# Optimization experiments

Measured on AMD Instinct MI355X. Metric: run time of the kernel, lower is better.

The kernel has to match this reference:

```python
import jax, jax.numpy as jnp
import numpy as np

B, S, E = 2, 2048, 2048
H, HKV = 16, 4
G = H // HKV
QLR, KVLR = 1024, 512
DN, DR, DV = 128, 64, 128
DQK = DN + DR
EPS = 1.1920929e-07  # torch.finfo(float32).eps, F.rms_norm default


def rms_norm(x):
    return x * jax.lax.rsqrt(jnp.mean(x * x, axis=-1, keepdims=True) + EPS)


def apply_rope(x, cos, sin):
    # x: [B, S, h, D]; pairs are adjacent elements (torch view_as_complex convention)
    x0, x1 = x[..., 0::2], x[..., 1::2]            # [B,S,h,D/2]
    c = cos[None, :, None, :]
    s = sin[None, :, None, :]
    r0 = x0 * c - x1 * s
    r1 = x0 * s + x1 * c
    return jnp.stack([r0, r1], axis=-1).reshape(x.shape)


def setup_inputs() -> dict:
    key = jax.random.key(0)
    ks = jax.random.split(key, 8)
    inv_freq = 1.0 / (10000.0 ** (np.arange(0, DR, 2, dtype=np.float32) / DR))  # [DR/2]
    ang = np.arange(S, dtype=np.float32)[:, None] * inv_freq[None, :]           # [S, DR/2]
    return {
        "x": jax.random.normal(ks[0], (B, S, E), jnp.float32),
        "freqs_cos": jnp.asarray(np.cos(ang), jnp.float32),
        "freqs_sin": jnp.asarray(np.sin(ang), jnp.float32),
        "Wqa": jax.random.normal(ks[1], (QLR, E), jnp.float32) * (E ** -0.5),
        "Wqb": jax.random.normal(ks[2], (H * DQK, QLR), jnp.float32) * (QLR ** -0.5),
        "Wkva": jax.random.normal(ks[3], (KVLR + DR, E), jnp.float32) * (E ** -0.5),
        "Wkvb": jax.random.normal(ks[4], (HKV * (DN + DV), KVLR), jnp.float32) * (KVLR ** -0.5),
        "Wo": jax.random.normal(ks[5], (E, H * DV), jnp.float32) * ((H * DV) ** -0.5),
    }


def reference(x, freqs_cos, freqs_sin, Wqa, Wqb, Wkva, Wkvb, Wo):
    # Q path: low-rank down-proj -> rmsnorm -> up-proj
    q = rms_norm(x @ Wqa.T) @ Wqb.T                       # [B,S,H*DQK]
    q = q.reshape(B, S, H, DQK)
    q_nope, q_rope = q[..., :DN], q[..., DN:]
    q_rope = apply_rope(q_rope, freqs_cos, freqs_sin)
    q = jnp.concatenate([q_nope, q_rope], axis=-1)        # [B,S,H,DQK]

    # KV path: joint down-proj, shared rope key, up-proj of latent
    kv_a = x @ Wkva.T                                     # [B,S,KVLR+DR]
    kv_latent, k_rope = kv_a[..., :KVLR], kv_a[..., KVLR:]
    k_rope = jnp.broadcast_to(k_rope[:, :, None, :], (B, S, HKV, DR))
    k_rope = apply_rope(k_rope, freqs_cos, freqs_sin)     # [B,S,HKV,DR]
    kv = (rms_norm(kv_latent) @ Wkvb.T).reshape(B, S, HKV, DN + DV)
    k_nope, v = kv[..., :DN], kv[..., DN:]
    k = jnp.concatenate([k_nope, k_rope], axis=-1)        # [B,S,HKV,DQK]

    # GQA causal SDPA: group G query heads per kv head
    qg = q.reshape(B, S, HKV, G, DQK)
    scores = jnp.einsum("bsngd,btnd->bngst", qg, k) * (DQK ** -0.5)  # [B,HKV,G,S,S]
    causal = jnp.tril(jnp.ones((S, S), bool))
    scores = jnp.where(causal, scores, jnp.finfo(scores.dtype).min)
    attn = jax.nn.softmax(scores, axis=-1)
    o = jnp.einsum("bngst,btnd->bsngd", attn, v).reshape(B, S, H * DV)
    return o @ Wo.T                                        # [B,S,E]
```

## Files before the change

### kernel.cpp

```cpp
#include <hip/hip_runtime.h>
#include <cstdint>
#include <cstddef>

typedef __attribute__((ext_vector_type(4))) float f32x4;
typedef __attribute__((ext_vector_type(2))) float f32x2;
typedef __attribute__((ext_vector_type(8))) short short8;
typedef __attribute__((ext_vector_type(8))) __bf16 bf16x8;
typedef unsigned short u16;
typedef unsigned int u32;
typedef __attribute__((ext_vector_type(2))) unsigned int u32x2;
typedef __attribute__((ext_vector_type(4))) unsigned short u16x4;
typedef __attribute__((ext_vector_type(2))) unsigned short u16x2;

#define EPS_RMS 1.1920929e-07f

__device__ __forceinline__ u16 f2bf(float f) {
  union { float f; unsigned u; } v; v.f = f;
  unsigned r = v.u + 0x7FFFu + ((v.u >> 16) & 1u);
  return (u16)(r >> 16);
}
__device__ __forceinline__ float b2f(u16 x) {
  union { unsigned u; float f; } v; v.u = ((unsigned)x) << 16;
  return v.f;
}
__device__ __forceinline__ u32 cvt_pk_bf16(float lo, float hi) {
  u32 r;
  asm("v_cvt_pk_bf16_f32 %0, %1, %2" : "=v"(r) : "v"(lo), "v"(hi));
  return r;
}

template <typename V>
__device__ __forceinline__ auto mfma_try(V a, V b, f32x4 c, int)
    -> decltype(__builtin_amdgcn_mfma_f32_16x16x32_bf16(a, b, c, 0, 0, 0)) {
  return __builtin_amdgcn_mfma_f32_16x16x32_bf16(a, b, c, 0, 0, 0);
}
template <typename V>
__device__ __forceinline__ f32x4 mfma_try(V a, V b, f32x4 c, long) {
  return __builtin_amdgcn_mfma_f32_16x16x32_bf16(
      __builtin_bit_cast(bf16x8, a), __builtin_bit_cast(bf16x8, b), c, 0, 0, 0);
}
__device__ __forceinline__ f32x4 mfma_bf16(short8 a, short8 b, f32x4 c) {
  return mfma_try(a, b, c, 0);
}

__device__ __forceinline__ void load_lds16(u16* lds, const u16* g) {
  auto* gp = reinterpret_cast<const __attribute__((address_space(1))) unsigned int*>(
      reinterpret_cast<uintptr_t>(g));
  auto* lp = reinterpret_cast<__attribute__((address_space(3))) unsigned int*>(
      reinterpret_cast<uintptr_t>(lds));
  __builtin_amdgcn_global_load_lds(gp, lp, 16, 0, 0);
}

__device__ __forceinline__ float fast_exp2(float x) {
  return __builtin_amdgcn_exp2f(x);
}

template <int CTRL>
__device__ __forceinline__ float dpp_step(float v) {
  int t = __builtin_amdgcn_update_dpp(0, __builtin_bit_cast(int, v), CTRL, 0xF, 0xF, true);
  return __builtin_bit_cast(float, t);
}

__global__ __launch_bounds__(256) void cvt_all(const float* __restrict__ x,
                                               const float* __restrict__ Wqa,
                                               const float* __restrict__ Wkva,
                                               const float* __restrict__ Wqb,
                                               const float* __restrict__ Wkvb,
                                               const float* __restrict__ Wo,
                                               u16* __restrict__ xb,
                                               u16* __restrict__ wacat,
                                               u16* __restrict__ wqb,
                                               u16* __restrict__ wkvb,
                                               u16* __restrict__ wo) {
  const int blk = blockIdx.x;
  if (blk >= 8192 && blk < 11520) {
    int i = (blk - 8192) * 256 + threadIdx.x;
    int r = i >> 9;
    int c4 = i & 511;
    f32x4 v = {0.f, 0.f, 0.f, 0.f};
    if (r < 1024) v = ((const f32x4*)Wqa)[r * 512 + c4];
    else if (r < 1600) v = ((const f32x4*)Wkva)[(r - 1024) * 512 + c4];
    u16x4 o = {f2bf(v.x), f2bf(v.y), f2bf(v.z), f2bf(v.w)};
    ((u16x4*)wacat)[i] = o;
    return;
  }
  const float* src;
  u16* dst;
  int i;
  if (blk < 8192)       { i = blk * 256 + threadIdx.x;           src = x;    dst = xb;   }
  else if (blk < 14592) { i = (blk - 11520) * 256 + threadIdx.x; src = Wqb;  dst = wqb;  }
  else if (blk < 15104) { i = (blk - 14592) * 256 + threadIdx.x; src = Wkvb; dst = wkvb; }
  else                  { i = (blk - 15104) * 256 + threadIdx.x; src = Wo;   dst = wo;   }
  f32x4 v = ((const f32x4*)src)[i];
  u16x4 o = {f2bf(v.x), f2bf(v.y), f2bf(v.z), f2bf(v.w)};
  ((u16x4*)dst)[i] = o;
}

template <typename OutT, int EPI>
__device__ __forceinline__ void gemm_core(u16 (&As)[2][128 * 64],
                                          u16 (&Bs)[2][128 * 64],
                                          const u16* __restrict__ A,
                                          const u16* __restrict__ B,
                                          OutT* __restrict__ C,
                                          int N, int K, int gx, int nwg, int bid,
                                          const float* __restrict__ fc,
                                          const float* __restrict__ fs,
                                          u16* __restrict__ aux) {
  const int cpx = nwg >> 3;
  const int swz = (bid & 7) * cpx + (bid >> 3);
  const int by = swz / gx, bxx = swz - by * gx;
  const int tid = threadIdx.x;
  const int lane = tid & 63, w = tid >> 6;
  const int wr = w >> 1, wc = w & 1;
  const int l16 = lane & 15, lg = lane >> 4;
  const int row0 = by * 128, col0 = bxx * 128;

  const u16* Ab = A + (size_t)row0 * K;
  const u16* Bb = B + (size_t)col0 * K;

  f32x4 acc[4][4] = {};

  int soff[4], ldst[4];
#pragma unroll
  for (int j = 0; j < 4; ++j) {
    int c = j * 256 + tid;
    int row = c >> 3;
    int rb = (c & 7) << 4;
    int sb = rb ^ ((row & 7) << 4);
    soff[j] = row * K + (sb >> 1);
    ldst[j] = c * 8;
  }

#pragma unroll
  for (int j = 0; j < 4; ++j) load_lds16(As[0] + ldst[j], Ab + soff[j]);
#pragma unroll
  for (int j = 0; j < 4; ++j) load_lds16(Bs[0] + ldst[j], Bb + soff[j]);
  __syncthreads();

  int cur = 0;
  for (int k0 = 0; k0 < K; k0 += 64) {
    if (k0 + 64 < K) {
#pragma unroll
      for (int j = 0; j < 4; ++j) load_lds16(As[cur ^ 1] + ldst[j], Ab + soff[j] + k0 + 64);
#pragma unroll
      for (int j = 0; j < 4; ++j) load_lds16(Bs[cur ^ 1] + ldst[j], Bb + soff[j] + k0 + 64);
    }
    const u16* Ac = As[cur];
    const u16* Bc = Bs[cur];
    short8 a[2][4], bfr[2][4];
#pragma unroll
    for (int mt = 0; mt < 4; ++mt) {
      const int rowA = wr * 64 + mt * 16 + l16;
      const int sw = (rowA & 7) << 4;
#pragma unroll
      for (int kk = 0; kk < 2; ++kk)
        a[kk][mt] = *(const short8*)(Ac + rowA * 64 + (((kk * 64 + lg * 16) ^ sw) >> 1));
    }
#pragma unroll
    for (int nt = 0; nt < 4; ++nt) {
      const int rowB = wc * 64 + nt * 16 + l16;
      const int sw = (rowB & 7) << 4;
#pragma unroll
      for (int kk = 0; kk < 2; ++kk)
        bfr[kk][nt] = *(const short8*)(Bc + rowB * 64 + (((kk * 64 + lg * 16) ^ sw) >> 1));
    }
#pragma unroll
    for (int kk = 0; kk < 2; ++kk)
#pragma unroll
      for (int mt = 0; mt < 4; ++mt)
#pragma unroll
        for (int nt = 0; nt < 4; ++nt)
          acc[mt][nt] = mfma_bf16(a[kk][mt], bfr[kk][nt], acc[mt][nt]);
    __syncthreads();
    cur ^= 1;
  }

  if constexpr (EPI == 0 || EPI == 1) {
#pragma unroll
    for (int mt = 0; mt < 4; ++mt)
#pragma unroll
      for (int nt = 0; nt < 4; ++nt)
#pragma unroll
        for (int i = 0; i < 4; ++i) {
          int row = row0 + wr * 64 + mt * 16 + lg * 4 + i;
          int col = col0 + wc * 64 + nt * 16 + l16;
          if constexpr (EPI == 0)
            C[(size_t)row * N + col] = acc[mt][nt][i];
          else
            C[(size_t)row * N + col] = f2bf(acc[mt][nt][i]);
        }
  } else if constexpr (EPI == 2) {
    const float qscale = 0.07216878364870322f * 1.4426950408889634f;
#pragma unroll
    for (int mt = 0; mt < 4; ++mt)
#pragma unroll
      for (int nt = 0; nt < 4; ++nt) {
        int col = col0 + wc * 64 + nt * 16 + l16;
        int hh = ((col >> 6) * 43) >> 7;
        int cin = col - hh * 192;
        int m = (cin - 128) >> 1;
#pragma unroll
        for (int i = 0; i < 4; ++i) {
          int row = row0 + wr * 64 + mt * 16 + lg * 4 + i;
          int bb = row >> 11, ss = row & 2047;
          float v = acc[mt][nt][i];
          float pv = dpp_step<0xB1>(v);
          float val = v;
          if (cin >= 128) {
            float c = fc[ss * 32 + m], sn = fs[ss * 32 + m];
            val = ((l16 & 1) == 0) ? (v * c - pv * sn) : (pv * sn + v * c);
          }
          ((u16*)C)[((size_t)((bb * 16 + hh) * 2048 + ss)) * 192 + cin] = f2bf(val * qscale);
        }
      }
  } else {
#pragma unroll
    for (int mt = 0; mt < 4; ++mt)
#pragma unroll
      for (int nt = 0; nt < 4; ++nt) {
        int col = col0 + wc * 64 + nt * 16 + l16;
        int nn = col >> 8, cin = col & 255;
        int rowb = row0 + wr * 64 + mt * 16 + lg * 4;
        int bb = rowb >> 11, ss0 = rowb & 2047;
        if (cin < 128) {
#pragma unroll
          for (int i = 0; i < 4; ++i)
            ((u16*)C)[((size_t)((bb * 4 + nn) * 2048 + ss0 + i)) * 192 + cin] =
                f2bf(acc[mt][nt][i]);
        } else {
          int dv = cin - 128;
          u16x4 o = {f2bf(acc[mt][nt][0]), f2bf(acc[mt][nt][1]),
                     f2bf(acc[mt][nt][2]), f2bf(acc[mt][nt][3])};
          *(u16x4*)(aux + ((size_t)((bb * 4 + nn) * 128 + dv)) * 2048 + ss0) = o;
        }
      }
  }
}

template <typename OutT, int EPI>
__global__ __launch_bounds__(256) void gemm_bt(const u16* __restrict__ A,
                                               const u16* __restrict__ B,
                                               OutT* __restrict__ C,
                                               int N, int K, int gx,
                                               const float* __restrict__ fc,
                                               const float* __restrict__ fs,
                                               u16* __restrict__ aux) {
  __shared__ __align__(16) u16 As[2][128 * 64];
  __shared__ __align__(16) u16 Bs[2][128 * 64];
  gemm_core<OutT, EPI>(As, Bs, A, B, C, N, K, gx, gridDim.x, blockIdx.x,
                       fc, fs, aux);
}

__global__ __launch_bounds__(256) void gemm_g23(const u16* __restrict__ qlat,
                                                const u16* __restrict__ wqb,
                                                u16* __restrict__ qattn,
                                                const u16* __restrict__ kvlat,
                                                const u16* __restrict__ wkvb,
                                                u16* __restrict__ kattn,
                                                u16* __restrict__ vt,
                                                const float* __restrict__ fc,
                                                const float* __restrict__ fs) {
  __shared__ __align__(16) u16 As[2][128 * 64];
  __shared__ __align__(16) u16 Bs[2][128 * 64];
  if (blockIdx.x < 768) {
    gemm_core<u16, 2>(As, Bs, qlat, wqb, qattn, 3072, 1024, 24, 768,
                      blockIdx.x, fc, fs, nullptr);
  } else {
    gemm_core<u16, 3>(As, Bs, kvlat, wkvb, kattn, 1024, 512, 8, 256,
                      blockIdx.x - 768, nullptr, nullptr, vt);
  }
}

__global__ __launch_bounds__(256) void rms_fused(const u16* __restrict__ c1b,
                                                 const float* __restrict__ fc,
                                                 const float* __restrict__ fs,
                                                 u16* __restrict__ qlat,
                                                 u16* __restrict__ kvlat,
                                                 u16* __restrict__ Ka) {
  __shared__ float smq[4], smk[4];
  int t = blockIdx.x;
  const u16* row = c1b + (size_t)t * 1664;
  u16x4 v4u = ((const u16x4*)row)[threadIdx.x];
  u16x2 v2u = ((const u16x2*)(row + 1024))[threadIdx.x];
  float v4x = b2f(v4u.x), v4y = b2f(v4u.y), v4z = b2f(v4u.z), v4w = b2f(v4u.w);
  float v2x = b2f(v2u.x), v2y = b2f(v2u.y);
  float sq = v4x * v4x + v4y * v4y + v4z * v4z + v4w * v4w;
  float sk = v2x * v2x + v2y * v2y;
#pragma unroll
  for (int off = 32; off; off >>= 1) { sq += __shfl_xor(sq, off); sk += __shfl_xor(sk, off); }
  if ((threadIdx.x & 63) == 0) { smq[threadIdx.x >> 6] = sq; smk[threadIdx.x >> 6] = sk; }
  __syncthreads();
  float rq = rsqrtf((smq[0] + smq[1] + smq[2] + smq[3]) * (1.0f / 1024.0f) + EPS_RMS);
  float rk = rsqrtf((smk[0] + smk[1] + smk[2] + smk[3]) * (1.0f / 512.0f) + EPS_RMS);
  u16x4 oq = {f2bf(v4x * rq), f2bf(v4y * rq), f2bf(v4z * rq), f2bf(v4w * rq)};
  ((u16x4*)(qlat + (size_t)t * 1024))[threadIdx.x] = oq;
  u16x2 ok = {f2bf(v2x * rk), f2bf(v2y * rk)};
  ((u16x2*)(kvlat + (size_t)t * 512))[threadIdx.x] = ok;
  if (threadIdx.x < 32) {
    int bb = t >> 11, s = t & 2047;
    int m = threadIdx.x;
    float x0 = b2f(row[1536 + 2 * m]), x1 = b2f(row[1537 + 2 * m]);
    float c = fc[s * 32 + m], sn = fs[s * 32 + m];
    u16 r0 = f2bf(x0 * c - x1 * sn);
    u16 r1 = f2bf(x0 * sn + x1 * c);
#pragma unroll
    for (int nn = 0; nn < 4; ++nn) {
      size_t base = ((size_t)((bb * 4 + nn) * 2048 + s)) * 192 + 128;
      Ka[base + 2 * m] = r0;
      Ka[base + 2 * m + 1] = r1;
    }
  }
}

__global__ __launch_bounds__(256, 2) void attn_kernel(const u16* __restrict__ Qa,
                                                      const u16* __restrict__ Ka,
                                                      const u16* __restrict__ VTp,
                                                      u16* __restrict__ Ob) {
  __shared__ __align__(16) u16 Ks[64 * 192];
  __shared__ __align__(16) u16 Vs[128 * 64];
  __shared__ __align__(16) u32 Ppk[4][32][36];
  const int gid = blockIdx.x;
  const int bx = (gid < 256) ? (15 - (gid >> 5)) : ((gid - 256) >> 5);
  const int hb = gid & 31;
  const int b = hb >> 4;
  const int h = hb & 15;
  const int n = h >> 2;
  const int tid = threadIdx.x;
  const int lane = tid & 63;
  const int w = tid >> 6;
  const int l16 = lane & 15;
  const int lg = lane >> 4;

  const u16* Qp = Qa + ((size_t)((b * 16 + h) * 2048 + bx * 128 + w * 32)) * 192;
  const u16* Kp = Ka + ((size_t)((b * 4 + n) * 2048)) * 192;
  const u16* Vp = VTp + ((size_t)((b * 4 + n) * 128)) * 2048;

  int oK[6];
#pragma unroll
  for (int j = 0; j < 6; ++j) {
    int c = j * 256 + tid;
    int row = (c * 2731) >> 16;
    int rb = (c - row * 24) << 4;
    int sb = rb ^ ((row & 7) << 4);
    oK[j] = row * 192 + (sb >> 1);
  }
  int oV[4];
#pragma unroll
  for (int j = 0; j < 4; ++j) {
    int c = j * 256 + tid;
    int row = c >> 3;
    int rb = (c & 7) << 4;
    int sb = rb ^ ((row & 7) << 4);
    oV[j] = row * 2048 + (sb >> 1);
  }

  short8 qf[2][6];
#pragma unroll
  for (int g = 0; g < 2; ++g)
#pragma unroll
    for (int kc = 0; kc < 6; ++kc)
      qf[g][kc] = *(const short8*)(Qp + (size_t)(g * 16 + l16) * 192 + kc * 32 + lg * 8);

  float mrow[2], lrow[2];
  f32x4 oacc[2][8];
#pragma unroll
  for (int g = 0; g < 2; ++g) { mrow[g] = -1e30f; lrow[g] = 0.f; }
#pragma unroll
  for (int g = 0; g < 2; ++g)
#pragma unroll
    for (int vb = 0; vb < 8; ++vb) oacc[g][vb] = (f32x4){0.f, 0.f, 0.f, 0.f};

  const int wrow = bx * 128 + w * 32;
  const int NT = 2 * bx + 2;

  f32x4 kreg[6], vreg[4];
#pragma unroll
  for (int j = 0; j < 6; ++j) kreg[j] = *(const f32x4*)(Kp + oK[j]);
#pragma unroll
  for (int j = 0; j < 4; ++j) vreg[j] = *(const f32x4*)(Vp + oV[j]);

  for (int kt = 0; kt < NT; ++kt) {
    const int kb = kt * 64;
    __syncthreads();
#pragma unroll
    for (int j = 0; j < 6; ++j) *(f32x4*)(Ks + (j * 256 + tid) * 8) = kreg[j];
#pragma unroll
    for (int j = 0; j < 4; ++j) *(f32x4*)(Vs + (j * 256 + tid) * 8) = vreg[j];
    __syncthreads();
    if (kt + 1 < NT) {
      const int kb2 = kb + 64;
#pragma unroll
      for (int j = 0; j < 6; ++j)
        kreg[j] = *(const f32x4*)(Kp + oK[j] + (size_t)kb2 * 192);
#pragma unroll
      for (int j = 0; j < 4; ++j)
        vreg[j] = *(const f32x4*)(Vp + oV[j] + kb2);
    }
    if (kb > wrow + 31) continue;

    f32x4 sc[2][4];
#pragma unroll
    for (int g = 0; g < 2; ++g)
#pragma unroll
      for (int kn = 0; kn < 4; ++kn) sc[g][kn] = (f32x4){0.f, 0.f, 0.f, 0.f};
    __builtin_amdgcn_s_setprio(1);
#pragma unroll
    for (int kn = 0; kn < 4; ++kn) {
      const int rk = kn * 16 + l16;
      const u16* kbase = Ks + rk * 192;
      const int sw = (rk & 7) << 4;
#pragma unroll
      for (int kc = 0; kc < 6; ++kc) {
        short8 kf = *(const short8*)(kbase + (((kc * 64 + lg * 16) ^ sw) >> 1));
        sc[0][kn] = mfma_bf16(kf, qf[0][kc], sc[0][kn]);
        sc[1][kn] = mfma_bf16(kf, qf[1][kc], sc[1][kn]);
      }
    }
    __builtin_amdgcn_s_setprio(0);
    if (kb + 63 > wrow) {
#pragma unroll
      for (int g = 0; g < 2; ++g) {
        const int qabs = wrow + g * 16 + l16;
#pragma unroll
        for (int kn = 0; kn < 4; ++kn)
#pragma unroll
          for (int i = 0; i < 4; ++i)
            if (kb + kn * 16 + lg * 4 + i > qabs) sc[g][kn][i] = -1e30f;
      }
    }
    float pmax[2];
    int need = 0;
#pragma unroll
    for (int g = 0; g < 2; ++g) {
      float v = -1e30f;
#pragma unroll
      for (int kn = 0; kn < 4; ++kn)
        v = fmaxf(v, fmaxf(fmaxf(sc[g][kn][0], sc[g][kn][1]),
                           fmaxf(sc[g][kn][2], sc[g][kn][3])));
      v = fmaxf(v, __shfl_xor(v, 16));
      v = fmaxf(v, __shfl_xor(v, 32));
      pmax[g] = v;
      need |= (v > mrow[g] + 8.0f) ? 1 : 0;
    }
    if (__any(need)) {
#pragma unroll
      for (int g = 0; g < 2; ++g) {
        float mn = fmaxf(mrow[g], pmax[g]);
        float al = fast_exp2(mrow[g] - mn);
        mrow[g] = mn;
        lrow[g] *= al;
#pragma unroll
        for (int i = 0; i < 4; ++i) {
          float alq = __shfl(al, lg * 4 + i);
#pragma unroll
          for (int vb = 0; vb < 8; ++vb) oacc[g][vb][i] *= alq;
        }
      }
    }
#pragma unroll
    for (int g = 0; g < 2; ++g) {
      float rs = 0.f;
#pragma unroll
      for (int kn = 0; kn < 4; ++kn)
#pragma unroll
        for (int i = 0; i < 4; ++i) {
          float p = fast_exp2(sc[g][kn][i] - mrow[g]);
          sc[g][kn][i] = p;
          rs += p;
        }
      rs += __shfl_xor(rs, 16);
      rs += __shfl_xor(rs, 32);
      lrow[g] += rs;
    }
#pragma unroll
    for (int g = 0; g < 2; ++g) {
      const int r = g * 16 + l16;
#pragma unroll
      for (int kn = 0; kn < 4; ++kn) {
        u32x2 pk = {cvt_pk_bf16(sc[g][kn][0], sc[g][kn][1]),
                    cvt_pk_bf16(sc[g][kn][2], sc[g][kn][3])};
        *(u32x2*)&Ppk[w][r][kn * 8 + 2 * lg] = pk;
      }
    }
    short8 pa[2][2];
#pragma unroll
    for (int g = 0; g < 2; ++g) {
      const int r = g * 16 + l16;
      pa[g][0] = *(const short8*)&Ppk[w][r][lg * 4];
      pa[g][1] = *(const short8*)&Ppk[w][r][16 + lg * 4];
    }
    __builtin_amdgcn_s_setprio(1);
#pragma unroll
    for (int vb = 0; vb < 8; ++vb) {
      const int rv = vb * 16 + l16;
      const u16* vbase = Vs + rv * 64;
      const int swv = (rv & 7) << 4;
      short8 v0 = *(const short8*)(vbase + (((lg * 16) ^ swv) >> 1));
      short8 v1 = *(const short8*)(vbase + (((64 + lg * 16) ^ swv) >> 1));
      oacc[0][vb] = mfma_bf16(pa[0][0], v0, oacc[0][vb]);
      oacc[1][vb] = mfma_bf16(pa[1][0], v0, oacc[1][vb]);
      oacc[0][vb] = mfma_bf16(pa[0][1], v1, oacc[0][vb]);
      oacc[1][vb] = mfma_bf16(pa[1][1], v1, oacc[1][vb]);
    }
    __builtin_amdgcn_s_setprio(0);
  }
#pragma unroll
  for (int g = 0; g < 2; ++g) {
    float inv = 1.0f / lrow[g];
#pragma unroll
    for (int i = 0; i < 4; ++i) {
      float invq = __shfl(inv, lg * 4 + i);
      int srow = wrow + g * 16 + lg * 4 + i;
      size_t base = ((size_t)(b * 2048 + srow)) * 2048 + h * 128;
#pragma unroll
      for (int vb = 0; vb < 8; ++vb)
        Ob[base + vb * 16 + l16] = f2bf(oacc[g][vb][i] * invq);
    }
  }
}

extern "C" void kernel_launch(void* const* d_in, const int* in_sizes, int n_in,
                              void* d_out, int out_size, void* d_ws, size_t ws_size,
                              hipStream_t stream) {
  const float* x = (const float*)d_in[0];
  const float* fc = (const float*)d_in[1];
  const float* fs = (const float*)d_in[2];
  const float* Wqa = (const float*)d_in[3];
  const float* Wqb = (const float*)d_in[4];
  const float* Wkva = (const float*)d_in[5];
  const float* Wkvb = (const float*)d_in[6];
  const float* Wo = (const float*)d_in[7];
  float* out = (float*)d_out;

  char* ws = (char*)d_ws;
  u16* xb    = (u16*)(ws + 0);
  u16* wacat = (u16*)(ws + 16777216);
  u16* wqb   = (u16*)(ws + 23592960);
  u16* wkvb  = (u16*)(ws + 29884416);
  u16* wo    = (u16*)(ws + 30932992);
  u16* c1b   = (u16*)(ws + 39321600);
  u16* qlat  = (u16*)(ws + 52953088);
  u16* kvlat = (u16*)(ws + 61341696);
  u16* obf   = (u16*)(ws + 65536000);
  u16* qattn = (u16*)(ws + 82313216);
  u16* kattn = (u16*)(ws + 107479040);
  u16* vt    = (u16*)(ws + 113770496);
  if (ws_size < 117964800u) return;

  cvt_all<<<19200, 256, 0, stream>>>(x, Wqa, Wkva, Wqb, Wkvb, Wo,
                                     xb, wacat, wqb, wkvb, wo);

  gemm_bt<u16, 1><<<416, 256, 0, stream>>>(xb, wacat, c1b, 1664, 2048, 13,
                                           nullptr, nullptr, nullptr);
  rms_fused<<<4096, 256, 0, stream>>>(c1b, fc, fs, qlat, kvlat, kattn);
  gemm_g23<<<1024, 256, 0, stream>>>(qlat, wqb, qattn, kvlat, wkvb, kattn, vt,
                                     fc, fs);
  attn_kernel<<<512, 256, 0, stream>>>(qattn, kattn, vt, obf);
  gemm_bt<float, 0><<<512, 256, 0, stream>>>(obf, wo, out, 2048, 2048, 16,
                                             nullptr, nullptr, nullptr);
}
```

Before: 228.5 us.

## Overlap later weight conversions with first GEMM in a combined launch

Splits the fp32-to-bf16 conversion so only x, Wqa and Wkva are converted before the first projection GEMM. The Wqb, Wkvb and Wo conversions move into extra blocks of the GEMM launch, so that memory-bound conversion work can run alongside the compute-bound GEMM tiles. The combined kernel carries the GEMM's LDS allocation for the conversion blocks too, which may limit how many of them are resident at once. Block scheduling order also affects how much real overlap happens.

```diff
diff --git a/kernel.cpp b/kernel.cpp
--- a/kernel.cpp
+++ b/kernel.cpp
@@ -61,19 +61,18 @@
   return __builtin_bit_cast(float, t);
 }
 
-__global__ __launch_bounds__(256) void cvt_all(const float* __restrict__ x,
-                                               const float* __restrict__ Wqa,
-                                               const float* __restrict__ Wkva,
-                                               const float* __restrict__ Wqb,
-                                               const float* __restrict__ Wkvb,
-                                               const float* __restrict__ Wo,
-                                               u16* __restrict__ xb,
-                                               u16* __restrict__ wacat,
-                                               u16* __restrict__ wqb,
-                                               u16* __restrict__ wkvb,
-                                               u16* __restrict__ wo) {
+__global__ __launch_bounds__(256) void cvt_xw(const float* __restrict__ x,
+                                              const float* __restrict__ Wqa,
+                                              const float* __restrict__ Wkva,
+                                              u16* __restrict__ xb,
+                                              u16* __restrict__ wacat) {
   const int blk = blockIdx.x;
-  if (blk >= 8192 && blk < 11520) {
+  if (blk < 8192) {
+    int i = blk * 256 + threadIdx.x;
+    f32x4 v = ((const f32x4*)x)[i];
+    u16x4 o = {f2bf(v.x), f2bf(v.y), f2bf(v.z), f2bf(v.w)};
+    ((u16x4*)xb)[i] = o;
+  } else {
     int i = (blk - 8192) * 256 + threadIdx.x;
     int r = i >> 9;
     int c4 = i & 511;
@@ -82,18 +81,7 @@
     else if (r < 1600) v = ((const f32x4*)Wkva)[(r - 1024) * 512 + c4];
     u16x4 o = {f2bf(v.x), f2bf(v.y), f2bf(v.z), f2bf(v.w)};
     ((u16x4*)wacat)[i] = o;
-    return;
-  }
-  const float* src;
-  u16* dst;
-  int i;
-  if (blk < 8192)       { i = blk * 256 + threadIdx.x;           src = x;    dst = xb;   }
-  else if (blk < 14592) { i = (blk - 11520) * 256 + threadIdx.x; src = Wqb;  dst = wqb;  }
-  else if (blk < 15104) { i = (blk - 14592) * 256 + threadIdx.x; src = Wkvb; dst = wkvb; }
-  else                  { i = (blk - 15104) * 256 + threadIdx.x; src = Wo;   dst = wo;   }
-  f32x4 v = ((const f32x4*)src)[i];
-  u16x4 o = {f2bf(v.x), f2bf(v.y), f2bf(v.z), f2bf(v.w)};
-  ((u16x4*)dst)[i] = o;
+  }
 }
 
 template <typename OutT, int EPI>
@@ -251,6 +239,35 @@
                        fc, fs, aux);
 }
 
+__global__ __launch_bounds__(256) void gemm_g1w(const u16* __restrict__ xb,
+                                                const u16* __restrict__ wacat,
+                                                u16* __restrict__ c1b,
+                                                const float* __restrict__ Wqb,
+                                                const float* __restrict__ Wkvb,
+                                                const float* __restrict__ Wo,
+                                                u16* __restrict__ wqb,
+                                                u16* __restrict__ wkvb,
+                                                u16* __restrict__ wo) {
+  __shared__ __align__(16) u16 As[2][128 * 64];
+  __shared__ __align__(16) u16 Bs[2][128 * 64];
+  const int blk = blockIdx.x;
+  if (blk < 416) {
+    gemm_core<u16, 1>(As, Bs, xb, wacat, c1b, 1664, 2048, 13, 416, blk,
+                      nullptr, nullptr, nullptr);
+    return;
+  }
+  const int cb = blk - 416;
+  const float* src;
+  u16* dst;
+  int i;
+  if (cb < 3072)      { i = cb * 256 + threadIdx.x;          src = Wqb;  dst = wqb;  }
+  else if (cb < 3584) { i = (cb - 3072) * 256 + threadIdx.x; src = Wkvb; dst = wkvb; }
+  else                { i = (cb - 3584) * 256 + threadIdx.x; src = Wo;   dst = wo;   }
+  f32x4 v = ((const f32x4*)src)[i];
+  u16x4 o = {f2bf(v.x), f2bf(v.y), f2bf(v.z), f2bf(v.w)};
+  ((u16x4*)dst)[i] = o;
+}
+
 __global__ __launch_bounds__(256) void gemm_g23(const u16* __restrict__ qlat,
                                                 const u16* __restrict__ wqb,
                                                 u16* __restrict__ qattn,
@@ -547,11 +564,10 @@
   u16* vt    = (u16*)(ws + 113770496);
   if (ws_size < 117964800u) return;
 
-  cvt_all<<<19200, 256, 0, stream>>>(x, Wqa, Wkva, Wqb, Wkvb, Wo,
-                                     xb, wacat, wqb, wkvb, wo);
-
-  gemm_bt<u16, 1><<<416, 256, 0, stream>>>(xb, wacat, c1b, 1664, 2048, 13,
-                                           nullptr, nullptr, nullptr);
+  cvt_xw<<<11520, 256, 0, stream>>>(x, Wqa, Wkva, xb, wacat);
+
+  gemm_g1w<<<8096, 256, 0, stream>>>(xb, wacat, c1b, Wqb, Wkvb, Wo,
+                                     wqb, wkvb, wo);
   rms_fused<<<4096, 256, 0, stream>>>(c1b, fc, fs, qlat, kvlat, kattn);
   gemm_g23<<<1024, 256, 0, stream>>>(qlat, wqb, qattn, kvlat, wkvb, kattn, vt,
                                      fc, fs);
```

Result: no change. 225.7 us (-1.3%).
